# Optimization experiments

Measured on AMD Instinct MI355X. Metric: run time of the kernel, lower is better.

## Reference

```python
import jax, jax.numpy as jnp
import numpy as np

B, P, N, D = 128, 2048, 256, 2

def setup_inputs() -> dict:
    key = jax.random.key(0)
    k1, k2, k3 = jax.random.split(key, 3)
    batch = jax.random.normal(k1, (B, P, D), dtype=jnp.float32)
    not_dummy = jnp.ones((B, P), dtype=jnp.float32)
    centers = jax.random.uniform(k2, (N, D), dtype=jnp.float32)
    sharpness = jax.random.uniform(k3, (N, D), dtype=jnp.float32)
    exponent = jnp.ones((1,), dtype=jnp.float32)
    return {"batch": batch, "not_dummy": not_dummy, "centers": centers,
            "sharpness": sharpness, "exponent": exponent}

def reference(batch, not_dummy, centers, sharpness, exponent):
    # batch: (B, P, D); centers/sharpness: (N, D); exponent: (1,)
    # weighted L1 distance from each point to each structure element: (B, N, P)
    diff = jnp.abs(centers[None, :, None, :] - batch[:, None, :, :])
    s = jnp.sum(diff * jnp.abs(sharpness)[None, :, None, :], axis=-1)
    # rational kernel, mask out dummy (padding) points, sum-pool over points
    r = 1.0 / (1.0 + s ** exponent[0])
    r = r * not_dummy[:, None, :]
    return jnp.sum(r, axis=-1)  # (B, N)
```

## Files before the change

kernel.cpp:

```cpp
#include <hip/hip_runtime.h>

constexpr int B   = 128;
constexpr int P   = 2048;
constexpr int N   = 256;
constexpr int TPB = 256;
constexpr int NPB = 8;
constexpr int KQ  = 4;

__device__ __forceinline__ float rdfl(float v) {
    return __int_as_float(__builtin_amdgcn_readfirstlane(__float_as_int(v)));
}

__global__ __launch_bounds__(TPB, 8)
void SLayerRational_43190191128606_kernel(
    const float* __restrict__ batch,
    const float* __restrict__ not_dummy,
    const float* __restrict__ centers,
    const float* __restrict__ sharpness,
    const float* __restrict__ exponent,
    float* __restrict__ out)
{
    const int b    = blockIdx.x >> 5;
    const int n0   = (blockIdx.x & 31) * NPB;
    const int wave = threadIdx.x >> 6;
    const int lane = threadIdx.x & 63;

    float c0[NPB], c1[NPB], a0[NPB], a1[NPB];
#pragma unroll
    for (int c = 0; c < NPB; ++c) {
        c0[c] = rdfl(centers[(n0 + c) * 2 + 0]);
        c1[c] = rdfl(centers[(n0 + c) * 2 + 1]);
        a0[c] = rdfl(fabsf(sharpness[(n0 + c) * 2 + 0]));
        a1[c] = rdfl(fabsf(sharpness[(n0 + c) * 2 + 1]));
    }
    const float e = exponent[0];

    float acc[NPB];
#pragma unroll
    for (int c = 0; c < NPB; ++c) acc[c] = 0.0f;

    if (e == 1.0f) {
        const float4* bb4 = reinterpret_cast<const float4*>(batch)
                          + (size_t)b * (P / 2) + wave * 256;
        const float2* nd2 = reinterpret_cast<const float2*>(not_dummy)
                          + (size_t)b * (P / 2) + wave * 256;

        float4 xq[KQ];
        float2 wq[KQ];
#pragma unroll
        for (int k = 0; k < KQ; ++k) {
            xq[k] = bb4[k * 64 + lane];
            wq[k] = nd2[k * 64 + lane];
        }

#pragma unroll
        for (int c = 0; c < NPB; ++c) {
#pragma unroll
            for (int k = 0; k < KQ; ++k) {
                const float4 x = xq[k];
                const float2 w = wq[k];
                const float ua = fmaf(fabsf(c0[c] - x.x), a0[c],
                                  fmaf(fabsf(c1[c] - x.y), a1[c], 1.0f));
                const float ub = fmaf(fabsf(c0[c] - x.z), a0[c],
                                  fmaf(fabsf(c1[c] - x.w), a1[c], 1.0f));
                float num = w.x * ub;
                num = fmaf(w.y, ua, num);
                const float den = ua * ub;
                acc[c] = fmaf(num, __builtin_amdgcn_rcpf(den), acc[c]);
            }
        }
    } else {
        const float2* bb = reinterpret_cast<const float2*>(batch)
                         + (size_t)b * P + wave * 512;
        const float*  nd = not_dummy + (size_t)b * P + wave * 512;
        for (int it = 0; it < 8; ++it) {
            const int p = it * 64 + lane;
            const float2 x = bb[p];
            const float  w = nd[p];
#pragma unroll
            for (int c = 0; c < NPB; ++c) {
                const float s = fmaf(fabsf(c0[c] - x.x), a0[c],
                                     fabsf(c1[c] - x.y) * a1[c]);
                acc[c] += w / (1.0f + powf(s, e));
            }
        }
    }

    const bool lo = (lane < 32);
    float r[4];
#pragma unroll
    for (int j = 0; j < 4; ++j) {
        const float m = lo ? acc[j] : acc[j + 4];
        const float o = lo ? acc[j + 4] : acc[j];
        r[j] = m + __shfl_xor(o, 32, 64);
    }
#pragma unroll
    for (int j = 0; j < 4; ++j) {
#pragma unroll
        for (int off = 16; off > 0; off >>= 1)
            r[j] += __shfl_xor(r[j], off, 64);
    }

    __shared__ float red[4][NPB];
    if ((lane & 31) == 0) {
        float4* dst = reinterpret_cast<float4*>(&red[wave][(lane >> 5) * 4]);
        *dst = make_float4(r[0], r[1], r[2], r[3]);
    }
    __syncthreads();

    if (threadIdx.x < NPB) {
        const int t = threadIdx.x;
        out[b * N + n0 + t] = red[0][t] + red[1][t] + red[2][t] + red[3][t];
    }
}

extern "C" void kernel_launch(void* const* d_in, const int* in_sizes, int n_in,
                              void* d_out, int out_size, void* d_ws, size_t ws_size,
                              hipStream_t stream) {
    const float* batch     = (const float*)d_in[0];
    const float* not_dummy = (const float*)d_in[1];
    const float* centers   = (const float*)d_in[2];
    const float* sharpness = (const float*)d_in[3];
    const float* exponent  = (const float*)d_in[4];
    float* out = (float*)d_out;

    const int blocks = B * (N / NPB);
    SLayerRational_43190191128606_kernel<<<blocks, TPB, 0, stream>>>(
        batch, not_dummy, centers, sharpness, exponent, out);
}
```

Before: 20.30 us.

## Compute rational kernel in packed fp16 and double elements per block

The e==1 fast path now converts points, weights, centers and sharpness to packed half2 and computes the distance, reciprocal and weighted accumulation with packed fp16 math, summing each element's four-point partials in fp16 before converting to float. Elements per block grow from 8 to 16, which halves the block count and amortizes the per-block point loads and reductions. The aim is to roughly double ALU throughput and cut the dependency on the fp32 reciprocal. It trades accuracy for speed: inputs near ±4 with sharpness up to 1 lose precision in fp16, and the partial sums accumulate in half.

```diff
diff --git a/kernel.cpp b/kernel.cpp
--- a/kernel.cpp
+++ b/kernel.cpp
@@ -1,14 +1,21 @@
 #include <hip/hip_runtime.h>
+#include <hip/hip_fp16.h>
 
 constexpr int B   = 128;
 constexpr int P   = 2048;
 constexpr int N   = 256;
 constexpr int TPB = 256;
-constexpr int NPB = 8;
+constexpr int NPB = 16;
 constexpr int KQ  = 4;
 
 __device__ __forceinline__ float rdfl(float v) {
     return __int_as_float(__builtin_amdgcn_readfirstlane(__float_as_int(v)));
+}
+__device__ __forceinline__ __half2 rdfl2(__half2 v) {
+    union { __half2 h; int i; } u;
+    u.h = v;
+    u.i = __builtin_amdgcn_readfirstlane(u.i);
+    return u.h;
 }
 
 __global__ __launch_bounds__(TPB, 8)
@@ -20,56 +27,67 @@
     const float* __restrict__ exponent,
     float* __restrict__ out)
 {
-    const int b    = blockIdx.x >> 5;
-    const int n0   = (blockIdx.x & 31) * NPB;
+    const int b    = blockIdx.x >> 4;
+    const int n0   = (blockIdx.x & 15) * NPB;
     const int wave = threadIdx.x >> 6;
     const int lane = threadIdx.x & 63;
 
-    float c0[NPB], c1[NPB], a0[NPB], a1[NPB];
-#pragma unroll
-    for (int c = 0; c < NPB; ++c) {
-        c0[c] = rdfl(centers[(n0 + c) * 2 + 0]);
-        c1[c] = rdfl(centers[(n0 + c) * 2 + 1]);
-        a0[c] = rdfl(fabsf(sharpness[(n0 + c) * 2 + 0]));
-        a1[c] = rdfl(fabsf(sharpness[(n0 + c) * 2 + 1]));
-    }
     const float e = exponent[0];
 
     float acc[NPB];
-#pragma unroll
-    for (int c = 0; c < NPB; ++c) acc[c] = 0.0f;
 
     if (e == 1.0f) {
+        __half2 C0[NPB], C1[NPB], A0[NPB], A1[NPB];
+#pragma unroll
+        for (int c = 0; c < NPB; ++c) {
+            C0[c] = rdfl2(__float2half2_rn(centers[(n0 + c) * 2 + 0]));
+            C1[c] = rdfl2(__float2half2_rn(centers[(n0 + c) * 2 + 1]));
+            A0[c] = rdfl2(__float2half2_rn(fabsf(sharpness[(n0 + c) * 2 + 0])));
+            A1[c] = rdfl2(__float2half2_rn(fabsf(sharpness[(n0 + c) * 2 + 1])));
+        }
+
         const float4* bb4 = reinterpret_cast<const float4*>(batch)
                           + (size_t)b * (P / 2) + wave * 256;
         const float2* nd2 = reinterpret_cast<const float2*>(not_dummy)
                           + (size_t)b * (P / 2) + wave * 256;
 
-        float4 xq[KQ];
-        float2 wq[KQ];
+        __half2 X0[KQ], X1[KQ], W[KQ];
 #pragma unroll
         for (int k = 0; k < KQ; ++k) {
-            xq[k] = bb4[k * 64 + lane];
-            wq[k] = nd2[k * 64 + lane];
+            const float4 x = bb4[k * 64 + lane];
+            const float2 w = nd2[k * 64 + lane];
+            X0[k] = __floats2half2_rn(x.x, x.z);
+            X1[k] = __floats2half2_rn(x.y, x.w);
+            W[k]  = __floats2half2_rn(w.x, w.y);
         }
+
+        const __half2 one2 = __float2half2_rn(1.0f);
 
 #pragma unroll
         for (int c = 0; c < NPB; ++c) {
+            __half2 ah = __float2half2_rn(0.0f);
 #pragma unroll
             for (int k = 0; k < KQ; ++k) {
-                const float4 x = xq[k];
-                const float2 w = wq[k];
-                const float ua = fmaf(fabsf(c0[c] - x.x), a0[c],
-                                  fmaf(fabsf(c1[c] - x.y), a1[c], 1.0f));
-                const float ub = fmaf(fabsf(c0[c] - x.z), a0[c],
-                                  fmaf(fabsf(c1[c] - x.w), a1[c], 1.0f));
-                float num = w.x * ub;
-                num = fmaf(w.y, ua, num);
-                const float den = ua * ub;
-                acc[c] = fmaf(num, __builtin_amdgcn_rcpf(den), acc[c]);
+                const __half2 d0 = __hsub2(C0[c], X0[k]);
+                const __half2 d1 = __hsub2(C1[c], X1[k]);
+                const __half2 u  = __hfma2(__habs2(d0), A0[c],
+                                   __hfma2(__habs2(d1), A1[c], one2));
+                ah = __hfma2(W[k], h2rcp(u), ah);
             }
+            acc[c] = __low2float(ah) + __high2float(ah);
         }
     } else {
+        float c0[NPB], c1[NPB], a0[NPB], a1[NPB];
+#pragma unroll
+        for (int c = 0; c < NPB; ++c) {
+            c0[c] = rdfl(centers[(n0 + c) * 2 + 0]);
+            c1[c] = rdfl(centers[(n0 + c) * 2 + 1]);
+            a0[c] = rdfl(fabsf(sharpness[(n0 + c) * 2 + 0]));
+            a1[c] = rdfl(fabsf(sharpness[(n0 + c) * 2 + 1]));
+        }
+#pragma unroll
+        for (int c = 0; c < NPB; ++c) acc[c] = 0.0f;
+
         const float2* bb = reinterpret_cast<const float2*>(batch)
                          + (size_t)b * P + wave * 512;
         const float*  nd = not_dummy + (size_t)b * P + wave * 512;
@@ -87,15 +105,15 @@
     }
 
     const bool lo = (lane < 32);
-    float r[4];
+    float r[8];
 #pragma unroll
-    for (int j = 0; j < 4; ++j) {
-        const float m = lo ? acc[j] : acc[j + 4];
-        const float o = lo ? acc[j + 4] : acc[j];
+    for (int j = 0; j < 8; ++j) {
+        const float m = lo ? acc[j] : acc[j + 8];
+        const float o = lo ? acc[j + 8] : acc[j];
         r[j] = m + __shfl_xor(o, 32, 64);
     }
 #pragma unroll
-    for (int j = 0; j < 4; ++j) {
+    for (int j = 0; j < 8; ++j) {
 #pragma unroll
         for (int off = 16; off > 0; off >>= 1)
             r[j] += __shfl_xor(r[j], off, 64);
@@ -103,8 +121,9 @@
 
     __shared__ float red[4][NPB];
     if ((lane & 31) == 0) {
-        float4* dst = reinterpret_cast<float4*>(&red[wave][(lane >> 5) * 4]);
-        *dst = make_float4(r[0], r[1], r[2], r[3]);
+        float4* dst = reinterpret_cast<float4*>(&red[wave][(lane >> 5) * 8]);
+        dst[0] = make_float4(r[0], r[1], r[2], r[3]);
+        dst[1] = make_float4(r[4], r[5], r[6], r[7]);
     }
     __syncthreads();
 
```

Measured after the change: 24.57 us. 21.0% more time.
